# Optimization experiments

Hardware: AMD Instinct MI355X
Metric: run time of the kernel (lower is better)

## Reference

```python
import jax, jax.numpy as jnp
import numpy as np

HS = 1024          # hidden_size
NH_ATTN = 16       # attention heads
NH_LACT = 4        # lact fast-weight heads
DIN = HS // NH_LACT  # 256
DH = DIN             # inter_multi = 1
CHUNK = 1024       # lact_chunk_size
EPS = 1e-5


def setup_inputs() -> dict:
    key = jax.random.key(0)
    ks = jax.random.split(key, 6)
    B, S = 1, 4096
    x = jax.random.normal(ks[0], (B, S, HS), jnp.float32)
    ln_w = jnp.ones((HS,), jnp.float32)
    ln_b = jnp.zeros((HS,), jnp.float32)
    in_proj_w = jax.random.normal(ks[1], (3 * HS, HS), jnp.float32) * (HS ** -0.5)
    in_proj_b = jnp.zeros((3 * HS,), jnp.float32)
    out_proj_w = jax.random.normal(ks[2], (HS, HS), jnp.float32) * (HS ** -0.5)
    out_proj_b = jnp.zeros((HS,), jnp.float32)
    w0 = jax.random.normal(ks[3], (NH_LACT, DH, DIN), jnp.float32) / np.sqrt(DIN)
    w1 = jax.random.normal(ks[4], (NH_LACT, DIN, DH), jnp.float32) / np.sqrt(DH)
    w2 = jax.random.normal(ks[5], (NH_LACT, DH, DIN), jnp.float32) / np.sqrt(DIN)
    return dict(x=x, ln_w=ln_w, ln_b=ln_b, in_proj_w=in_proj_w, in_proj_b=in_proj_b,
                out_proj_w=out_proj_w, out_proj_b=out_proj_b, w0=w0, w1=w1, w2=w2)


def reference(x, ln_w, ln_b, in_proj_w, in_proj_b, out_proj_w, out_proj_b, w0, w1, w2):
    B, S, D = x.shape
    # LayerNorm
    mu = jnp.mean(x, axis=-1, keepdims=True)
    var = jnp.var(x, axis=-1, keepdims=True)
    xn = (x - mu) * jax.lax.rsqrt(var + EPS) * ln_w + ln_b

    # --- torch nn.MultiheadAttention(batch_first=True), self-attention, no mask ---
    qkv = xn @ in_proj_w.T + in_proj_b                      # [B,S,3D]
    q, k, v = jnp.split(qkv, 3, axis=-1)
    hd = D // NH_ATTN
    def heads(t):
        return t.reshape(B, S, NH_ATTN, hd).transpose(0, 2, 1, 3)  # [B,H,S,hd]
    q = heads(q) * (hd ** -0.5)
    k = heads(k)
    v = heads(v)
    attn = jax.nn.softmax(jnp.einsum('bhqd,bhkd->bhqk', q, k), axis=-1)
    ao = jnp.einsum('bhqk,bhkd->bhqd', attn, v).transpose(0, 2, 1, 3).reshape(B, S, D)
    attn_out = ao @ out_proj_w.T + out_proj_b

    # --- chunked fast-weight SwiGLU TTT (block_causal_lact_swiglu) ---
    # q=k=v=chunk; lr0=lr1=lr2=1; each outer chunk is one TTT step starting from
    # the module parameters: update weights on (k,v) then apply to q (block-causal).
    nc = S // CHUNK
    c = xn.reshape(B, nc, CHUNK, NH_LACT, DIN).transpose(0, 1, 3, 2, 4)  # [B,nc,nh,C,din]
    kv = c  # k == v == q == chunk

    # fast-weight SwiGLU forward on keys: f(k) = w1 @ (silu(w0 k) * (w2 k))
    gate = jnp.einsum('bnhcd,hed->bnhce', kv, w0)     # [B,nc,nh,C,dh]
    sg = jax.nn.sigmoid(gate)
    h = gate * sg                                     # silu
    g = jnp.einsum('bnhcd,hed->bnhce', kv, w2)
    hidden = h * g

    # negative dot-product loss L = -sum(v * f(k)) -> dOut = -v
    dout = -kv                                        # [B,nc,nh,C,din]
    dhid = jnp.einsum('bnhcd,hde->bnhce', dout, w1)
    dh = dhid * g
    dg = dhid * h
    dpre = dh * (sg + gate * sg * (1.0 - sg))         # silu'
    dw1 = jnp.einsum('bnhcd,bnhce->bnhde', dout, hidden)
    dw0 = jnp.einsum('bnhce,bnhcd->bnhed', dpre, kv)
    dw2 = jnp.einsum('bnhce,bnhcd->bnhed', dg, kv)

    # SGD step (lr = 1)
    w0n = w0 - dw0   # [B,nc,nh,dh,din]
    w1n = w1 - dw1
    w2n = w2 - dw2

    # apply updated fast weights to queries
    gq = jnp.einsum('bnhcd,bnhed->bnhce', c, w0n)
    hq = gq * jax.nn.sigmoid(gq)
    gq2 = jnp.einsum('bnhcd,bnhed->bnhce', c, w2n)
    oq = jnp.einsum('bnhce,bnhde->bnhcd', hq * gq2, w1n)  # [B,nc,nh,C,din]
    lact_out = oq.transpose(0, 1, 3, 2, 4).reshape(B, S, D)

    return lact_out + attn_out
```

## Files before the change

kernel.cpp:

```cpp
#include <hip/hip_runtime.h>
#include <hip/hip_bf16.h>


typedef __bf16 bf16_t;
typedef __bf16 bf16x8 __attribute__((ext_vector_type(8)));
typedef __bf16 bf16x4 __attribute__((ext_vector_type(4)));
typedef float  f32x4  __attribute__((ext_vector_type(4)));
typedef float  f32x16 __attribute__((ext_vector_type(16)));

#define SW64(r,cg) ((cg) ^ ((r)&7))
#define SW32(r,cg) ((cg) ^ (((r)>>2)&3))

static __device__ __forceinline__ f32x4 mfma16(bf16x8 a, bf16x8 b, f32x4 c){
  return __builtin_amdgcn_mfma_f32_16x16x32_bf16(a, b, c, 0, 0, 0);
}
static __device__ __forceinline__ f32x16 mfma32(bf16x8 a, bf16x8 b, f32x16 c){
  return __builtin_amdgcn_mfma_f32_32x32x16_bf16(a, b, c, 0, 0, 0);
}
__device__ __forceinline__ float sigm(float x){ return 1.0f/(1.0f + __expf(-x)); }
static __device__ __forceinline__ unsigned pkbf(float lo, float hi){
  unsigned short a = __builtin_bit_cast(unsigned short, (__bf16)lo);
  unsigned short b = __builtin_bit_cast(unsigned short, (__bf16)hi);
  return (unsigned)a | ((unsigned)b<<16);
}

__global__ __launch_bounds__(256) void ln_kernel(const float* __restrict__ x,
    const float* __restrict__ w, const float* __restrict__ b,
    bf16_t* __restrict__ xnb)
{
  int s = blockIdx.x, t = threadIdx.x;
  const float4* xr = (const float4*)(x + (size_t)s*1024);
  float4 v = xr[t];
  float sum = v.x+v.y+v.z+v.w;
  float ss  = v.x*v.x+v.y*v.y+v.z*v.z+v.w*v.w;
  #pragma unroll
  for (int o=32;o>0;o>>=1){ sum += __shfl_down(sum,o); ss += __shfl_down(ss,o); }
  __shared__ float red[8];
  __shared__ float stats[2];
  int wid=t>>6, lane=t&63;
  if(lane==0){ red[wid]=sum; red[4+wid]=ss; }
  __syncthreads();
  if(t==0){
    float S0=red[0]+red[1]+red[2]+red[3];
    float Q0=red[4]+red[5]+red[6]+red[7];
    float mu=S0*(1.0f/1024.0f);
    float var=Q0*(1.0f/1024.0f)-mu*mu;
    stats[0]=mu; stats[1]=rsqrtf(var+1e-5f);
  }
  __syncthreads();
  float mu=stats[0], rs=stats[1];
  float4 wv=((const float4*)w)[t], bv=((const float4*)b)[t];
  float4 o;
  o.x=(v.x-mu)*rs*wv.x+bv.x;
  o.y=(v.y-mu)*rs*wv.y+bv.y;
  o.z=(v.z-mu)*rs*wv.z+bv.z;
  o.w=(v.w-mu)*rs*wv.w+bv.w;
  bf16x4 ob = { (bf16_t)o.x, (bf16_t)o.y, (bf16_t)o.z, (bf16_t)o.w };
  *(bf16x4*)&xnb[(size_t)s*1024 + t*4] = ob;
}

__global__ __launch_bounds__(256) void prep_weights(
  const float* __restrict__ ipw, const float* __restrict__ opw,
  const float* __restrict__ w0, const float* __restrict__ w2,
  const float* __restrict__ w1,
  bf16_t* __restrict__ ipwb, bf16_t* __restrict__ opwb,
  bf16_t* __restrict__ w0b, bf16_t* __restrict__ w2b, bf16_t* __restrict__ w1tb)
{
  long i = ((long)blockIdx.x*256 + threadIdx.x)*4;
  if (i < 3145728) {
    float4 v = *(const float4*)(ipw + i);
    bf16x4 o = {(bf16_t)v.x,(bf16_t)v.y,(bf16_t)v.z,(bf16_t)v.w};
    *(bf16x4*)&ipwb[i] = o;
  } else if (i < 4194304) {
    long j = i - 3145728;
    float4 v = *(const float4*)(opw + j);
    bf16x4 o = {(bf16_t)v.x,(bf16_t)v.y,(bf16_t)v.z,(bf16_t)v.w};
    *(bf16x4*)&opwb[j] = o;
  } else if (i < 4456448) {
    long j = i - 4194304;
    float4 v = *(const float4*)(w0 + j);
    bf16x4 o = {(bf16_t)v.x,(bf16_t)v.y,(bf16_t)v.z,(bf16_t)v.w};
    *(bf16x4*)&w0b[j] = o;
  } else if (i < 4718592) {
    long j = i - 4456448;
    float4 v = *(const float4*)(w2 + j);
    bf16x4 o = {(bf16_t)v.x,(bf16_t)v.y,(bf16_t)v.z,(bf16_t)v.w};
    *(bf16x4*)&w2b[j] = o;
  } else if (i < 4980736) {
    long j = i - 4718592;
    int h = (int)(j>>16), rem = (int)(j&65535), d = rem>>8, e0 = rem&255;
    float4 v = *(const float4*)(w1 + j);
    bf16_t* dst = w1tb + h*65536 + d;
    dst[(e0+0)*256] = (bf16_t)v.x;
    dst[(e0+1)*256] = (bf16_t)v.y;
    dst[(e0+2)*256] = (bf16_t)v.z;
    dst[(e0+3)*256] = (bf16_t)v.w;
  }
}

__global__ __launch_bounds__(256) void xnT_kernel(const bf16_t* __restrict__ xnb,
                                                  bf16_t* __restrict__ xt)
{
  int dt = blockIdx.x, ct = blockIdx.y, bz = blockIdx.z;
  int nb = bz>>2, hb = bz&3;
  int t = threadIdx.x;
  __shared__ __align__(16) bf16_t T[4096];
  int r = t>>2, seg = t&3;
  const bf16_t* src = xnb + ((size_t)nb*1024 + ct*64 + r)*1024 + hb*256 + dt*64 + seg*16;
  uint4 a0 = *(const uint4*)src;
  uint4 a1 = *(const uint4*)(src + 8);
  *(uint4*)&T[r*64 + ((((seg*2  )&7)^(r&7))<<3)] = a0;
  *(uint4*)&T[r*64 + ((((seg*2+1)&7)^(r&7))<<3)] = a1;
  __syncthreads();
  int d = t>>2, s2 = t&3;
  unsigned uu[8];
  #pragma unroll
  for (int p=0;p<8;p++){
    int c0 = s2*16 + 2*p, c1 = c0+1;
    unsigned short e0 = __builtin_bit_cast(unsigned short,
        T[c0*64 + (((d>>3)^(c0&7))<<3) + (d&7)]);
    unsigned short e1 = __builtin_bit_cast(unsigned short,
        T[c1*64 + (((d>>3)^(c1&7))<<3) + (d&7)]);
    uu[p] = (unsigned)e0 | ((unsigned)e1<<16);
  }
  uint4 o0 = {uu[0],uu[1],uu[2],uu[3]}, o1 = {uu[4],uu[5],uu[6],uu[7]};
  bf16_t* dst = xt + (size_t)bz*262144 + (size_t)(dt*64 + d)*1024 + ct*64 + s2*16;
  *(uint4*)dst = o0;
  *(uint4*)(dst+8) = o1;
}

template<int EPI>
__global__ __launch_bounds__(256) void gemm_mfma(
  const bf16_t* __restrict__ Ag, const bf16_t* __restrict__ Bg,
  float* __restrict__ Cg, const float* __restrict__ bias,
  bf16_t* __restrict__ O1, bf16_t* __restrict__ O2, bf16_t* __restrict__ O3,
  int M, int N, int K, int lda, int ldb, int ldc,
  long oAn, long oAh, long oBn, long oBh, long oCn, long oCh)
{
  int bz = blockIdx.z, nb = bz>>2, hb = bz&3;
  const bf16_t* A = Ag + (long)nb*oAn + (long)hb*oAh;
  const bf16_t* B = Bg + (long)nb*oBn + (long)hb*oBh;
  int m0 = blockIdx.y<<7, n0 = blockIdx.x<<7;
  int t = threadIdx.x, l = t&63, w = t>>6;
  int wr = w>>1, wc = w&1;
  __shared__ __align__(16) bf16_t As[4096], Bs[4096];
  f32x4 acc[4][4];
  #pragma unroll
  for (int i=0;i<4;i++)
    #pragma unroll
    for (int j=0;j<4;j++){ f32x4 z={0.f,0.f,0.f,0.f}; acc[i][j]=z; }

  int r0 = t>>2, c0 = t&3, r1 = r0+64;
  const bf16_t* Arow0 = A + (size_t)(m0+r0)*lda + c0*8;
  const bf16_t* Arow1 = A + (size_t)(m0+r1)*lda + c0*8;
  const bf16_t* Brow0 = B + (size_t)(n0+r0)*ldb + c0*8;
  const bf16_t* Brow1 = B + (size_t)(n0+r1)*ldb + c0*8;
  uint4 av0 = *(const uint4*)Arow0, av1 = *(const uint4*)Arow1;
  uint4 bv0 = *(const uint4*)Brow0, bv1 = *(const uint4*)Brow1;
  int wo0 = r0*32 + (SW32(r0,c0)<<3), wo1 = r1*32 + (SW32(r1,c0)<<3);

  for (int k0=0; k0<K; k0+=32) {
    if (k0) __syncthreads();
    *(uint4*)&As[wo0] = av0; *(uint4*)&As[wo1] = av1;
    *(uint4*)&Bs[wo0] = bv0; *(uint4*)&Bs[wo1] = bv1;
    __syncthreads();
    if (k0+32 < K) {
      av0 = *(const uint4*)(Arow0 + k0+32); av1 = *(const uint4*)(Arow1 + k0+32);
      bv0 = *(const uint4*)(Brow0 + k0+32); bv1 = *(const uint4*)(Brow1 + k0+32);
    }
    bf16x8 af[4], bb[4];
    #pragma unroll
    for (int mt=0;mt<4;mt++){
      int row = (wr<<6)+(mt<<4)+(l&15);
      af[mt] = *(bf16x8*)&As[row*32 + (SW32(row, (l>>4))<<3)];
    }
    #pragma unroll
    for (int nt=0;nt<4;nt++){
      int row = (wc<<6)+(nt<<4)+(l&15);
      bb[nt] = *(bf16x8*)&Bs[row*32 + (SW32(row, (l>>4))<<3)];
    }
    #pragma unroll
    for (int mt=0;mt<4;mt++)
      #pragma unroll
      for (int nt=0;nt<4;nt++)
        acc[mt][nt] = mfma16(af[mt], bb[nt], acc[mt][nt]);
  }

  float* C = Cg + (long)nb*oCn + (long)hb*oCh;
  #pragma unroll
  for (int mt=0;mt<4;mt++){
    #pragma unroll
    for (int nt=0;nt<4;nt++){
      #pragma unroll
      for (int q=0;q<4;q++){
        int gr = m0 + (wr<<6) + (mt<<4) + ((l>>4)<<2) + q;
        int gc = n0 + (wc<<6) + (nt<<4) + (l&15);
        float v = acc[mt][nt][q];
        if constexpr (EPI==0) {
          C[(size_t)gr*ldc + gc] = v;
        } else if constexpr (EPI==1) {
          C[(size_t)gr*ldc + gc] = v + bias[gc];
        } else if constexpr (EPI==2) {
          C[(size_t)gr*ldc + gc] += v;
        } else if constexpr (EPI==3) {
          v += bias[gc];
          int seg = gc>>10, c2 = gc&1023, hh = c2>>6, dd = c2&63;
          size_t oi = ((size_t)hh*4096 + gr)*64 + dd;
          if (seg==0)      O1[oi] = (bf16_t)(v*0.18033688011112042f);
          else if (seg==1) O2[oi] = (bf16_t)v;
          else             O3[oi] = (bf16_t)v;
        } else {
          float pv = bias[(long)hb*65536 + (size_t)gr*256 + gc];
          float r = (EPI==4) ? (pv + v) : (pv - v);
          O1[(long)bz*65536 + (size_t)gr*256 + gc] = (bf16_t)r;
        }
      }
    }
  }
}

__global__ __launch_bounds__(256) void vtrans(const bf16_t* __restrict__ Vb,
                                              bf16_t* __restrict__ Vt)
{
  int st = blockIdx.x, h = blockIdx.y, t = threadIdx.x;
  __shared__ __align__(16) bf16_t T[64*72];
  #pragma unroll
  for (int G=t; G<512; G+=256) {
    int r = G>>3, cg = G&7;
    *(uint4*)&T[r*72 + cg*8] =
      *(const uint4*)(Vb + ((size_t)h*4096 + st*64 + r)*64 + cg*8);
  }
  __syncthreads();
  int d = t>>2, seg = t&3;
  bf16x8 e0, e1;
  #pragma unroll
  for (int i=0;i<8;i++)  e0[i] = T[(seg*16+i)*72 + d];
  #pragma unroll
  for (int i=0;i<8;i++)  e1[i] = T[(seg*16+8+i)*72 + d];
  size_t base = ((size_t)h*64 + d)*4096 + st*64 + seg*16;
  *(bf16x8*)(Vt + base)     = e0;
  *(bf16x8*)(Vt + base + 8) = e1;
}

__global__ __launch_bounds__(256,2) void attn_mfma2(
    const bf16_t* __restrict__ Qb, const bf16_t* __restrict__ Kb,
    const bf16_t* __restrict__ Vt, bf16_t* __restrict__ ao)
{
  int h = blockIdx.x, qblk = blockIdx.y;
  int t = threadIdx.x, w = t>>6, l = t&63;
  int lh = l>>5, lq = l&31;
  __shared__ __align__(16) bf16_t Ks[4096], Vs[4096];

  const bf16_t* Kg = Kb + (size_t)h*4096*64;
  const bf16_t* Vg = Vt + (size_t)h*64*4096;

  bf16x8 qf[4];
  {
    const bf16_t* Qg = Qb + ((size_t)h*4096 + (size_t)qblk*128 + w*32 + lq)*64 + lh*8;
    #pragma unroll
    for (int s=0;s<4;s++) qf[s] = *(const bf16x8*)(Qg + s*16);
  }

  int r0 = t>>3, c0 = t&7, r1 = r0+32;
  uint4 kv0 = *(const uint4*)(Kg + (size_t)r0*64 + c0*8);
  uint4 kv1 = *(const uint4*)(Kg + (size_t)r1*64 + c0*8);
  uint4 vv0 = *(const uint4*)(Vg + (size_t)r0*4096 + c0*8);
  uint4 vv1 = *(const uint4*)(Vg + (size_t)r1*4096 + c0*8);

  float m_r = -1e30f, l_r = 0.f;
  f32x16 Oa, Ob;
  #pragma unroll
  for (int i=0;i<16;i++){ Oa[i]=0.f; Ob[i]=0.f; }

  int wo0 = r0*64 + (SW64(r0,c0)<<3);
  int wo1 = r1*64 + (SW64(r1,c0)<<3);

  for (int kt=0; kt<64; ++kt) {
    __syncthreads();
    *(uint4*)&Ks[wo0] = kv0;
    *(uint4*)&Ks[wo1] = kv1;
    *(uint4*)&Vs[wo0] = vv0;
    *(uint4*)&Vs[wo1] = vv1;
    __syncthreads();
    if (kt < 63) {
      const bf16_t* Kg2 = Kg + (size_t)(kt+1)*4096;
      kv0 = *(const uint4*)(Kg2 + (size_t)r0*64 + c0*8);
      kv1 = *(const uint4*)(Kg2 + (size_t)r1*64 + c0*8);
      const bf16_t* Vg2 = Vg + (kt+1)*64;
      vv0 = *(const uint4*)(Vg2 + (size_t)r0*4096 + c0*8);
      vv1 = *(const uint4*)(Vg2 + (size_t)r1*4096 + c0*8);
    }
    f32x16 S0, S1;
    #pragma unroll
    for (int i=0;i<16;i++){ S0[i]=0.f; S1[i]=0.f; }
    #pragma unroll
    for (int s=0;s<4;s++){
      int g = (s<<1) + lh;
      bf16x8 k0 = *(const bf16x8*)&Ks[lq*64 + (SW64(lq,g)<<3)];
      int rowb = 32 + lq;
      bf16x8 k1 = *(const bf16x8*)&Ks[rowb*64 + (SW64(rowb,g)<<3)];
      S0 = mfma32(k0, qf[s], S0);
      S1 = mfma32(k1, qf[s], S1);
    }
    float mx = S0[0];
    #pragma unroll
    for (int i=1;i<16;i++) mx = fmaxf(mx, S0[i]);
    #pragma unroll
    for (int i=0;i<16;i++) mx = fmaxf(mx, S1[i]);
    mx = fmaxf(mx, __shfl_xor(mx, 32));
    if (__any(mx > m_r + 8.0f)) {
      float mn = fmaxf(m_r, mx);
      float sc = exp2f(m_r - mn);
      l_r *= sc;
      m_r = mn;
      #pragma unroll
      for (int reg=0; reg<16; reg++){
        int row = (reg&3) + 8*(reg>>2) + 4*lh;
        float s_row = __shfl(sc, row);
        Oa[reg] *= s_row;
        Ob[reg] *= s_row;
      }
    }
    float rs = 0.f;
    #pragma unroll
    for (int i=0;i<16;i++){ float p = exp2f(S0[i]-m_r); S0[i]=p; rs+=p; }
    #pragma unroll
    for (int i=0;i<16;i++){ float p = exp2f(S1[i]-m_r); S1[i]=p; rs+=p; }
    rs += __shfl_xor(rs, 32);
    l_r += rs;
    unsigned pk0[4][2], pk1[4][2];
    #pragma unroll
    for (int u2=0; u2<4; u2++){
      #pragma unroll
      for (int wd=0; wd<2; wd++){
        int q0 = 4*u2 + 2*wd;
        pk0[u2][wd] = pkbf(S0[q0], S0[q0+1]);
        pk1[u2][wd] = pkbf(S1[q0], S1[q0+1]);
      }
    }
    #pragma unroll
    for (int ks=0; ks<4; ks++){
      int v0 = 2*(ks&1);
      unsigned x0, x1, y0, y1;
      if (ks < 2) { x0 = pk0[v0][0]; x1 = pk0[v0][1]; y0 = pk0[v0+1][0]; y1 = pk0[v0+1][1]; }
      else        { x0 = pk1[v0][0]; x1 = pk1[v0][1]; y0 = pk1[v0+1][0]; y1 = pk1[v0+1][1]; }
      asm volatile("v_permlane32_swap_b32 %0, %1" : "+v"(x0), "+v"(y0));
      asm volatile("v_permlane32_swap_b32 %0, %1" : "+v"(x1), "+v"(y1));
      uint4 pau = {x0, x1, y0, y1};
      bf16x8 pa = __builtin_bit_cast(bf16x8, pau);
      int g = (ks<<1) + lh;
      bf16x8 vf0 = *(const bf16x8*)&Vs[lq*64 + (SW64(lq,g)<<3)];
      int rowb = 32 + lq;
      bf16x8 vf1 = *(const bf16x8*)&Vs[rowb*64 + (SW64(rowb,g)<<3)];
      Oa = mfma32(pa, vf0, Oa);
      Ob = mfma32(pa, vf1, Ob);
    }
  }
  #pragma unroll
  for (int reg=0; reg<16; reg++){
    int row = (reg&3) + 8*(reg>>2) + 4*lh;
    float lr = __shfl(l_r, row);
    float inv = 1.0f/lr;
    int grow = qblk*128 + w*32 + row;
    size_t base = (size_t)grow*1024 + h*64;
    ao[base + lq]      = (bf16_t)(Oa[reg]*inv);
    ao[base + 32 + lq] = (bf16_t)(Ob[reg]*inv);
  }
}

__global__ __launch_bounds__(256) void ew1T_kernel(
    const float* __restrict__ b0, const float* __restrict__ b1,
    const float* __restrict__ b2,
    bf16_t* __restrict__ hT, bf16_t* __restrict__ pT, bf16_t* __restrict__ gT)
{
  int et = blockIdx.x, ct = blockIdx.y, bz = blockIdx.z;
  int t = threadIdx.x;
  __shared__ __align__(16) bf16_t Th[4096], Tp[4096], Tg[4096];
  int r = t>>2, seg = t&3;
  size_t base = (size_t)bz*262144 + (size_t)(ct*64 + r)*256 + et*64 + seg*16;
  unsigned ph[8], pp[8], pg[8];
  #pragma unroll
  for (int j=0;j<4;j++){
    float4 gate = *(const float4*)(b0 + base + j*4);
    float4 gg   = *(const float4*)(b1 + base + j*4);
    float4 dh   = *(const float4*)(b2 + base + j*4);
    float hid[4], dpre[4], dgv[4];
    #define EW(c,idx) { float sg=sigm(gate.c); float hs=gate.c*sg; hid[idx]=hs*gg.c; \
                        float nd=-dh.c; float dh_=nd*gg.c; \
                        dpre[idx]=dh_*(sg+gate.c*sg*(1.0f-sg)); dgv[idx]=nd*hs; }
    EW(x,0) EW(y,1) EW(z,2) EW(w,3)
    #undef EW
    ph[j*2  ] = pkbf(hid[0],  hid[1]);  ph[j*2+1] = pkbf(hid[2],  hid[3]);
    pp[j*2  ] = pkbf(dpre[0], dpre[1]); pp[j*2+1] = pkbf(dpre[2], dpre[3]);
    pg[j*2  ] = pkbf(dgv[0],  dgv[1]);  pg[j*2+1] = pkbf(dgv[2],  dgv[3]);
  }
  int g0 = ((seg*2  )&7)^(r&7), g1 = ((seg*2+1)&7)^(r&7);
  uint4 h0={ph[0],ph[1],ph[2],ph[3]}, h1={ph[4],ph[5],ph[6],ph[7]};
  uint4 p0={pp[0],pp[1],pp[2],pp[3]}, p1={pp[4],pp[5],pp[6],pp[7]};
  uint4 q0={pg[0],pg[1],pg[2],pg[3]}, q1={pg[4],pg[5],pg[6],pg[7]};
  *(uint4*)&Th[r*64 + (g0<<3)] = h0; *(uint4*)&Th[r*64 + (g1<<3)] = h1;
  *(uint4*)&Tp[r*64 + (g0<<3)] = p0; *(uint4*)&Tp[r*64 + (g1<<3)] = p1;
  *(uint4*)&Tg[r*64 + (g0<<3)] = q0; *(uint4*)&Tg[r*64 + (g1<<3)] = q1;
  __syncthreads();
  int e = t>>2, s2 = t&3;
  size_t obase = (size_t)bz*262144 + (size_t)(et*64 + e)*1024 + ct*64 + s2*16;
  #pragma unroll
  for (int tens=0; tens<3; tens++){
    const bf16_t* T = (tens==0)?Th:(tens==1)?Tp:Tg;
    bf16_t* dst = ((tens==0)?hT:(tens==1)?pT:gT) + obase;
    unsigned uu[8];
    #pragma unroll
    for (int p=0;p<8;p++){
      int c0 = s2*16 + 2*p, c1 = c0+1;
      unsigned short e0 = __builtin_bit_cast(unsigned short,
          T[c0*64 + (((e>>3)^(c0&7))<<3) + (e&7)]);
      unsigned short e1 = __builtin_bit_cast(unsigned short,
          T[c1*64 + (((e>>3)^(c1&7))<<3) + (e&7)]);
      uu[p] = (unsigned)e0 | ((unsigned)e1<<16);
    }
    uint4 o0 = {uu[0],uu[1],uu[2],uu[3]}, o1 = {uu[4],uu[5],uu[6],uu[7]};
    *(uint4*)dst = o0;
    *(uint4*)(dst+8) = o1;
  }
}

__global__ __launch_bounds__(256) void lact_ew2(const float* __restrict__ gq,
    const float* __restrict__ gq2, bf16_t* __restrict__ ub)
{
  int i=blockIdx.x*256+threadIdx.x;
  float4 a=((const float4*)gq)[i], b=((const float4*)gq2)[i];
  bf16x4 o;
  o[0]=(bf16_t)(a.x*sigm(a.x)*b.x);
  o[1]=(bf16_t)(a.y*sigm(a.y)*b.y);
  o[2]=(bf16_t)(a.z*sigm(a.z)*b.z);
  o[3]=(bf16_t)(a.w*sigm(a.w)*b.w);
  *(bf16x4*)&ub[(size_t)i*4]=o;
}

extern "C" void kernel_launch(void* const* d_in, const int* in_sizes, int n_in,
                              void* d_out, int out_size, void* d_ws, size_t ws_size,
                              hipStream_t stream) {
  const float* x          = (const float*)d_in[0];
  const float* ln_w       = (const float*)d_in[1];
  const float* ln_b       = (const float*)d_in[2];
  const float* in_proj_w  = (const float*)d_in[3];
  const float* in_proj_b  = (const float*)d_in[4];
  const float* out_proj_w = (const float*)d_in[5];
  const float* out_proj_b = (const float*)d_in[6];
  const float* w0         = (const float*)d_in[7];
  const float* w1         = (const float*)d_in[8];
  const float* w2         = (const float*)d_in[9];
  float* out = (float*)d_out;

  float* ws = (float*)d_ws;
  bf16_t* xnb  = (bf16_t*)(ws);
  bf16_t* Qb   = (bf16_t*)(ws + 2097152);
  bf16_t* Kb   = (bf16_t*)(ws + 4194304);
  float*  buf0 = ws + 6291456;
  float*  buf1 = ws + 10485760;
  float*  buf2 = ws + 14680064;
  bf16_t* xnTb = (bf16_t*)(ws + 18874368);
  bf16_t* hTb  = (bf16_t*)(ws + 20971520);
  bf16_t* pTb  = (bf16_t*)(ws + 23068672);
  bf16_t* gTb  = (bf16_t*)(ws + 25165824);
  bf16_t* ipwb = (bf16_t*)(ws + 27262976);
  bf16_t* opwb = (bf16_t*)(ws + 28835840);
  bf16_t* w0b  = (bf16_t*)(ws + 29360128);
  bf16_t* w2b  = (bf16_t*)(ws + 29491200);
  bf16_t* w1tb = (bf16_t*)(ws + 29622272);
  bf16_t* w0nb = (bf16_t*)(ws + 29753344);
  bf16_t* w1nb = (bf16_t*)(ws + 30277632);
  bf16_t* w2nb = (bf16_t*)(ws + 30801920);
  bf16_t* Vb   = (bf16_t*)buf0;
  bf16_t* aob  = (bf16_t*)buf1;
  bf16_t* Vtp  = (bf16_t*)buf2;
  bf16_t* ub   = (bf16_t*)buf2;

  dim3 blk(256);

  ln_kernel<<<dim3(4096),blk,0,stream>>>(x, ln_w, ln_b, xnb);

  prep_weights<<<dim3(4864),blk,0,stream>>>(in_proj_w, out_proj_w, w0, w2, w1,
                                            ipwb, opwb, w0b, w2b, w1tb);

  gemm_mfma<3><<<dim3(24,32,1),blk,0,stream>>>(
      xnb, ipwb, nullptr, in_proj_b, Qb, Kb, Vb,
      4096,3072,1024, 1024,1024,0, 0,0,0,0,0,0);

  vtrans<<<dim3(64,16),blk,0,stream>>>(Vb, Vtp);

  attn_mfma2<<<dim3(16,32),blk,0,stream>>>(Qb, Kb, Vtp, aob);

  gemm_mfma<1><<<dim3(8,32,1),blk,0,stream>>>(
      aob, opwb, out, out_proj_b, nullptr,nullptr,nullptr,
      4096,1024,1024, 1024,1024,1024, 0,0,0,0,0,0);

  xnT_kernel<<<dim3(4,16,16),blk,0,stream>>>(xnb, xnTb);

  gemm_mfma<0><<<dim3(2,8,16),blk,0,stream>>>(
      xnb, w0b, buf0, nullptr, nullptr,nullptr,nullptr,
      1024,256,256, 1024,256,256, 1048576,256, 0,65536, 1048576,262144);
  gemm_mfma<0><<<dim3(2,8,16),blk,0,stream>>>(
      xnb, w2b, buf1, nullptr, nullptr,nullptr,nullptr,
      1024,256,256, 1024,256,256, 1048576,256, 0,65536, 1048576,262144);
  gemm_mfma<0><<<dim3(2,8,16),blk,0,stream>>>(
      xnb, w1tb, buf2, nullptr, nullptr,nullptr,nullptr,
      1024,256,256, 1024,256,256, 1048576,256, 0,65536, 1048576,262144);

  ew1T_kernel<<<dim3(4,16,16),blk,0,stream>>>(buf0, buf1, buf2, hTb, pTb, gTb);

  gemm_mfma<4><<<dim3(2,2,16),blk,0,stream>>>(
      xnTb, hTb, nullptr, w1, w1nb, nullptr,nullptr,
      256,256,1024, 1024,1024,0, 1048576,262144, 1048576,262144, 0,0);
  gemm_mfma<5><<<dim3(2,2,16),blk,0,stream>>>(
      pTb, xnTb, nullptr, w0, w0nb, nullptr,nullptr,
      256,256,1024, 1024,1024,0, 1048576,262144, 1048576,262144, 0,0);
  gemm_mfma<5><<<dim3(2,2,16),blk,0,stream>>>(
      gTb, xnTb, nullptr, w2, w2nb, nullptr,nullptr,
      256,256,1024, 1024,1024,0, 1048576,262144, 1048576,262144, 0,0);

  gemm_mfma<0><<<dim3(2,8,16),blk,0,stream>>>(
      xnb, w0nb, buf0, nullptr, nullptr,nullptr,nullptr,
      1024,256,256, 1024,256,256, 1048576,256, 262144,65536, 1048576,262144);
  gemm_mfma<0><<<dim3(2,8,16),blk,0,stream>>>(
      xnb, w2nb, buf1, nullptr, nullptr,nullptr,nullptr,
      1024,256,256, 1024,256,256, 1048576,256, 262144,65536, 1048576,262144);

  lact_ew2<<<dim3(4096),blk,0,stream>>>(buf0, buf1, ub);

  gemm_mfma<2><<<dim3(2,8,16),blk,0,stream>>>(
      ub, w1nb, out, nullptr, nullptr,nullptr,nullptr,
      1024,256,256, 256,256,1024, 1048576,262144, 262144,65536, 1048576,256);
}
```

Measured before the change: 448.8 us.

## Split attention over key halves with merge, batch LaCT GEMMs, fuse SwiGLU into final GEMM

Result: faster. 397.1 us (-11.5%).

```diff
diff --git a/kernel.cpp b/kernel.cpp
--- a/kernel.cpp
+++ b/kernel.cpp
@@ -22,6 +22,16 @@
   unsigned short a = __builtin_bit_cast(unsigned short, (__bf16)lo);
   unsigned short b = __builtin_bit_cast(unsigned short, (__bf16)hi);
   return (unsigned)a | ((unsigned)b<<16);
+}
+static __device__ __forceinline__ float hswap_max(float x){
+  float a=x, b=x;
+  asm volatile("v_permlane32_swap_b32 %0, %1" : "+v"(a), "+v"(b));
+  return fmaxf(a,b);
+}
+static __device__ __forceinline__ float hswap_add(float x){
+  float a=x, b=x;
+  asm volatile("v_permlane32_swap_b32 %0, %1" : "+v"(a), "+v"(b));
+  return a+b;
 }
 
 __global__ __launch_bounds__(256) void ln_kernel(const float* __restrict__ x,
@@ -129,34 +139,53 @@
   *(uint4*)(dst+8) = o1;
 }
 
-template<int EPI>
-__global__ __launch_bounds__(256) void gemm_mfma(
-  const bf16_t* __restrict__ Ag, const bf16_t* __restrict__ Bg,
-  float* __restrict__ Cg, const float* __restrict__ bias,
-  bf16_t* __restrict__ O1, bf16_t* __restrict__ O2, bf16_t* __restrict__ O3,
-  int M, int N, int K, int lda, int ldb, int ldc,
-  long oAn, long oAh, long oBn, long oBh, long oCn, long oCh)
-{
-  int bz = blockIdx.z, nb = bz>>2, hb = bz&3;
-  const bf16_t* A = Ag + (long)nb*oAn + (long)hb*oAh;
-  const bf16_t* B = Bg + (long)nb*oBn + (long)hb*oBh;
-  int m0 = blockIdx.y<<7, n0 = blockIdx.x<<7;
-  int t = threadIdx.x, l = t&63, w = t>>6;
-  int wr = w>>1, wc = w&1;
+template<bool AEW>
+__device__ __forceinline__ void gemm_core(
+    const bf16_t* __restrict__ A, const float* __restrict__ F0,
+    const float* __restrict__ F1, int lda,
+    const bf16_t* __restrict__ B, int ldb,
+    int K, int m0, int n0, f32x4 (&acc)[4][4])
+{
+  int t = threadIdx.x, l = t&63;
+  int w = t>>6, wr = w>>1, wc = w&1;
   __shared__ __align__(16) bf16_t As[4096], Bs[4096];
-  f32x4 acc[4][4];
-  #pragma unroll
-  for (int i=0;i<4;i++)
-    #pragma unroll
-    for (int j=0;j<4;j++){ f32x4 z={0.f,0.f,0.f,0.f}; acc[i][j]=z; }
-
   int r0 = t>>2, c0 = t&3, r1 = r0+64;
-  const bf16_t* Arow0 = A + (size_t)(m0+r0)*lda + c0*8;
-  const bf16_t* Arow1 = A + (size_t)(m0+r1)*lda + c0*8;
+  const bf16_t* Arow0 = nullptr; const bf16_t* Arow1 = nullptr;
+  const float *Fa0=nullptr,*Fa1=nullptr,*Fb0=nullptr,*Fb1=nullptr;
+  if constexpr (AEW) {
+    Fa0 = F0 + (size_t)(m0+r0)*lda + c0*8;
+    Fa1 = F0 + (size_t)(m0+r1)*lda + c0*8;
+    Fb0 = F1 + (size_t)(m0+r0)*lda + c0*8;
+    Fb1 = F1 + (size_t)(m0+r1)*lda + c0*8;
+  } else {
+    Arow0 = A + (size_t)(m0+r0)*lda + c0*8;
+    Arow1 = A + (size_t)(m0+r1)*lda + c0*8;
+  }
   const bf16_t* Brow0 = B + (size_t)(n0+r0)*ldb + c0*8;
   const bf16_t* Brow1 = B + (size_t)(n0+r1)*ldb + c0*8;
-  uint4 av0 = *(const uint4*)Arow0, av1 = *(const uint4*)Arow1;
-  uint4 bv0 = *(const uint4*)Brow0, bv1 = *(const uint4*)Brow1;
+
+  uint4 av0, av1, bv0, bv1;
+  auto loadA = [&](int k0, uint4& o0, uint4& o1){
+    if constexpr (AEW) {
+      float4 ga = *(const float4*)(Fa0 + k0), gb = *(const float4*)(Fa0 + k0 + 4);
+      float4 ha = *(const float4*)(Fb0 + k0), hb = *(const float4*)(Fb0 + k0 + 4);
+      o0.x = pkbf(ga.x*sigm(ga.x)*ha.x, ga.y*sigm(ga.y)*ha.y);
+      o0.y = pkbf(ga.z*sigm(ga.z)*ha.z, ga.w*sigm(ga.w)*ha.w);
+      o0.z = pkbf(gb.x*sigm(gb.x)*hb.x, gb.y*sigm(gb.y)*hb.y);
+      o0.w = pkbf(gb.z*sigm(gb.z)*hb.z, gb.w*sigm(gb.w)*hb.w);
+      float4 gc = *(const float4*)(Fa1 + k0), gd = *(const float4*)(Fa1 + k0 + 4);
+      float4 hc = *(const float4*)(Fb1 + k0), hd = *(const float4*)(Fb1 + k0 + 4);
+      o1.x = pkbf(gc.x*sigm(gc.x)*hc.x, gc.y*sigm(gc.y)*hc.y);
+      o1.y = pkbf(gc.z*sigm(gc.z)*hc.z, gc.w*sigm(gc.w)*hc.w);
+      o1.z = pkbf(gd.x*sigm(gd.x)*hd.x, gd.y*sigm(gd.y)*hd.y);
+      o1.w = pkbf(gd.z*sigm(gd.z)*hd.z, gd.w*sigm(gd.w)*hd.w);
+    } else {
+      o0 = *(const uint4*)(Arow0 + k0);
+      o1 = *(const uint4*)(Arow1 + k0);
+    }
+  };
+  loadA(0, av0, av1);
+  bv0 = *(const uint4*)Brow0; bv1 = *(const uint4*)Brow1;
   int wo0 = r0*32 + (SW32(r0,c0)<<3), wo1 = r1*32 + (SW32(r1,c0)<<3);
 
   for (int k0=0; k0<K; k0+=32) {
@@ -165,7 +194,7 @@
     *(uint4*)&Bs[wo0] = bv0; *(uint4*)&Bs[wo1] = bv1;
     __syncthreads();
     if (k0+32 < K) {
-      av0 = *(const uint4*)(Arow0 + k0+32); av1 = *(const uint4*)(Arow1 + k0+32);
+      loadA(k0+32, av0, av1);
       bv0 = *(const uint4*)(Brow0 + k0+32); bv1 = *(const uint4*)(Brow1 + k0+32);
     }
     bf16x8 af[4], bb[4];
@@ -185,38 +214,105 @@
       for (int nt=0;nt<4;nt++)
         acc[mt][nt] = mfma16(af[mt], bb[nt], acc[mt][nt]);
   }
-
-  float* C = Cg + (long)nb*oCn + (long)hb*oCh;
-  #pragma unroll
-  for (int mt=0;mt<4;mt++){
-    #pragma unroll
-    for (int nt=0;nt<4;nt++){
-      #pragma unroll
-      for (int q=0;q<4;q++){
-        int gr = m0 + (wr<<6) + (mt<<4) + ((l>>4)<<2) + q;
-        int gc = n0 + (wc<<6) + (nt<<4) + (l&15);
-        float v = acc[mt][nt][q];
-        if constexpr (EPI==0) {
-          C[(size_t)gr*ldc + gc] = v;
-        } else if constexpr (EPI==1) {
-          C[(size_t)gr*ldc + gc] = v + bias[gc];
-        } else if constexpr (EPI==2) {
-          C[(size_t)gr*ldc + gc] += v;
-        } else if constexpr (EPI==3) {
-          v += bias[gc];
-          int seg = gc>>10, c2 = gc&1023, hh = c2>>6, dd = c2&63;
-          size_t oi = ((size_t)hh*4096 + gr)*64 + dd;
-          if (seg==0)      O1[oi] = (bf16_t)(v*0.18033688011112042f);
-          else if (seg==1) O2[oi] = (bf16_t)v;
-          else             O3[oi] = (bf16_t)v;
-        } else {
-          float pv = bias[(long)hb*65536 + (size_t)gr*256 + gc];
-          float r = (EPI==4) ? (pv + v) : (pv - v);
-          O1[(long)bz*65536 + (size_t)gr*256 + gc] = (bf16_t)r;
-        }
-      }
-    }
-  }
+}
+
+#define EPILOOP(...) { int l=threadIdx.x&63, w_=threadIdx.x>>6, wr=w_>>1, wc=w_&1; \
+  _Pragma("unroll") for(int mt=0;mt<4;mt++) _Pragma("unroll") for(int nt=0;nt<4;nt++) \
+  _Pragma("unroll") for(int q=0;q<4;q++){ \
+    int gr=m0+(wr<<6)+(mt<<4)+((l>>4)<<2)+q; int gc=n0+(wc<<6)+(nt<<4)+(l&15); \
+    float v=acc[mt][nt][q]; __VA_ARGS__ } }
+
+#define ACCZERO f32x4 acc[4][4]; \
+  _Pragma("unroll") for(int i_=0;i_<4;i_++) _Pragma("unroll") for(int j_=0;j_<4;j_++){ \
+    f32x4 z_={0.f,0.f,0.f,0.f}; acc[i_][j_]=z_; }
+
+template<int EPI>
+__global__ __launch_bounds__(256) void gemm_big(
+  const bf16_t* __restrict__ A, const bf16_t* __restrict__ B,
+  float* __restrict__ C, const float* __restrict__ bias,
+  bf16_t* __restrict__ O1, bf16_t* __restrict__ O2, bf16_t* __restrict__ O3,
+  int K, int ldc)
+{
+  int m0 = blockIdx.y<<7, n0 = blockIdx.x<<7;
+  ACCZERO
+  gemm_core<false>(A, nullptr, nullptr, K, B, K, K, m0, n0, acc);
+  EPILOOP(
+    if constexpr (EPI==1) {
+      C[(size_t)gr*ldc + gc] = v + bias[gc];
+    } else {
+      v += bias[gc];
+      int seg = gc>>10; int c2 = gc&1023; int hh = c2>>6; int dd = c2&63;
+      size_t oi = ((size_t)hh*4096 + gr)*64 + dd;
+      if (seg==0)      O1[oi] = (bf16_t)(v*0.18033688011112042f);
+      else if (seg==1) O2[oi] = (bf16_t)v;
+      else             O3[oi] = (bf16_t)v;
+    }
+  )
+}
+
+__global__ __launch_bounds__(256) void lact_fwd(
+    const bf16_t* __restrict__ xnb,
+    const bf16_t* __restrict__ w0b, const bf16_t* __restrict__ w2b,
+    const bf16_t* __restrict__ w1tb,
+    float* __restrict__ b0, float* __restrict__ b1, float* __restrict__ b2)
+{
+  int bz = blockIdx.z, sel = blockIdx.x>>1;
+  const bf16_t* A = xnb + (size_t)(bz>>2)*1048576 + (size_t)(bz&3)*256;
+  const bf16_t* B = (sel==0?w0b:(sel==1?w2b:w1tb)) + (size_t)(bz&3)*65536;
+  float* C = (sel==0?b0:(sel==1?b1:b2)) + (size_t)bz*262144;
+  int m0 = blockIdx.y<<7, n0 = (blockIdx.x&1)<<7;
+  ACCZERO
+  gemm_core<false>(A, nullptr, nullptr, 1024, B, 256, 256, m0, n0, acc);
+  EPILOOP( C[(size_t)gr*256 + gc] = v; )
+}
+
+__global__ __launch_bounds__(256) void lact_apply(
+    const bf16_t* __restrict__ xnb,
+    const bf16_t* __restrict__ w0nb, const bf16_t* __restrict__ w2nb,
+    float* __restrict__ b0, float* __restrict__ b1)
+{
+  int bz = blockIdx.z, sel = blockIdx.x>>1;
+  const bf16_t* A = xnb + (size_t)(bz>>2)*1048576 + (size_t)(bz&3)*256;
+  const bf16_t* B = (sel? w2nb : w0nb) + (size_t)bz*65536;
+  float* C = (sel? b1 : b0) + (size_t)bz*262144;
+  int m0 = blockIdx.y<<7, n0 = (blockIdx.x&1)<<7;
+  ACCZERO
+  gemm_core<false>(A, nullptr, nullptr, 1024, B, 256, 256, m0, n0, acc);
+  EPILOOP( C[(size_t)gr*256 + gc] = v; )
+}
+
+__global__ __launch_bounds__(256) void lact_upd(
+    const bf16_t* __restrict__ xnTb, const bf16_t* __restrict__ hTb,
+    const bf16_t* __restrict__ pTb,  const bf16_t* __restrict__ gTb,
+    const float* __restrict__ w1, const float* __restrict__ w0,
+    const float* __restrict__ w2,
+    bf16_t* __restrict__ w1nb, bf16_t* __restrict__ w0nb, bf16_t* __restrict__ w2nb)
+{
+  int zz = blockIdx.z, sub = zz>>4, bz = zz&15, hb = bz&3;
+  const bf16_t* A = (sub==0? xnTb : (sub==1? pTb : gTb)) + (size_t)bz*262144;
+  const bf16_t* B = (sub==0? hTb : xnTb) + (size_t)bz*262144;
+  const float*  P = (sub==0? w1 : (sub==1? w0 : w2)) + (size_t)hb*65536;
+  bf16_t*       O = (sub==0? w1nb : (sub==1? w0nb : w2nb)) + (size_t)bz*65536;
+  float sgn = (sub==0) ? 1.0f : -1.0f;
+  int m0 = blockIdx.y<<7, n0 = blockIdx.x<<7;
+  ACCZERO
+  gemm_core<false>(A, nullptr, nullptr, 1024, B, 1024, 1024, m0, n0, acc);
+  EPILOOP( O[(size_t)gr*256 + gc] = (bf16_t)(P[(size_t)gr*256 + gc] + sgn*v); )
+}
+
+__global__ __launch_bounds__(256) void lact_final(
+    const float* __restrict__ gq, const float* __restrict__ gq2,
+    const bf16_t* __restrict__ w1nb, float* __restrict__ out)
+{
+  int bz = blockIdx.z;
+  const float* F0 = gq  + (size_t)bz*262144;
+  const float* F1 = gq2 + (size_t)bz*262144;
+  const bf16_t* B = w1nb + (size_t)bz*65536;
+  float* C = out + (size_t)(bz>>2)*1048576 + (size_t)(bz&3)*256;
+  int m0 = blockIdx.y<<7, n0 = (blockIdx.x&1)<<7;
+  ACCZERO
+  gemm_core<true>(nullptr, F0, F1, 256, B, 256, 256, m0, n0, acc);
+  EPILOOP( C[(size_t)gr*1024 + gc] += v; )
 }
 
 __global__ __launch_bounds__(256) void vtrans(const bf16_t* __restrict__ Vb,
@@ -242,17 +338,18 @@
   *(bf16x8*)(Vt + base + 8) = e1;
 }
 
-__global__ __launch_bounds__(256,2) void attn_mfma2(
+__global__ __launch_bounds__(256,4) void attn_mfma3(
     const bf16_t* __restrict__ Qb, const bf16_t* __restrict__ Kb,
-    const bf16_t* __restrict__ Vt, bf16_t* __restrict__ ao)
-{
-  int h = blockIdx.x, qblk = blockIdx.y;
+    const bf16_t* __restrict__ Vt, float* __restrict__ Opart,
+    float* __restrict__ mlpart)
+{
+  int h = blockIdx.x, qblk = blockIdx.y, z = blockIdx.z;
   int t = threadIdx.x, w = t>>6, l = t&63;
   int lh = l>>5, lq = l&31;
   __shared__ __align__(16) bf16_t Ks[4096], Vs[4096];
 
-  const bf16_t* Kg = Kb + (size_t)h*4096*64;
-  const bf16_t* Vg = Vt + (size_t)h*64*4096;
+  const bf16_t* Kg = Kb + (size_t)h*262144 + (size_t)z*131072;
+  const bf16_t* Vg = Vt + (size_t)h*262144 + (size_t)z*2048;
 
   bf16x8 qf[4];
   {
@@ -275,14 +372,14 @@
   int wo0 = r0*64 + (SW64(r0,c0)<<3);
   int wo1 = r1*64 + (SW64(r1,c0)<<3);
 
-  for (int kt=0; kt<64; ++kt) {
+  for (int kt=0; kt<32; ++kt) {
     __syncthreads();
     *(uint4*)&Ks[wo0] = kv0;
     *(uint4*)&Ks[wo1] = kv1;
     *(uint4*)&Vs[wo0] = vv0;
     *(uint4*)&Vs[wo1] = vv1;
     __syncthreads();
-    if (kt < 63) {
+    if (kt < 31) {
       const bf16_t* Kg2 = Kg + (size_t)(kt+1)*4096;
       kv0 = *(const uint4*)(Kg2 + (size_t)r0*64 + c0*8);
       kv1 = *(const uint4*)(Kg2 + (size_t)r1*64 + c0*8);
@@ -293,6 +390,7 @@
     f32x16 S0, S1;
     #pragma unroll
     for (int i=0;i<16;i++){ S0[i]=0.f; S1[i]=0.f; }
+    __builtin_amdgcn_s_setprio(1);
     #pragma unroll
     for (int s=0;s<4;s++){
       int g = (s<<1) + lh;
@@ -302,12 +400,14 @@
       S0 = mfma32(k0, qf[s], S0);
       S1 = mfma32(k1, qf[s], S1);
     }
-    float mx = S0[0];
-    #pragma unroll
-    for (int i=1;i<16;i++) mx = fmaxf(mx, S0[i]);
-    #pragma unroll
-    for (int i=0;i<16;i++) mx = fmaxf(mx, S1[i]);
-    mx = fmaxf(mx, __shfl_xor(mx, 32));
+    __builtin_amdgcn_s_setprio(0);
+    float mt_[8];
+    #pragma unroll
+    for (int i=0;i<8;i++) mt_[i] = fmaxf(fmaxf(S0[i],S0[i+8]), fmaxf(S1[i],S1[i+8]));
+    #pragma unroll
+    for (int i=0;i<4;i++) mt_[i] = fmaxf(mt_[i], mt_[i+4]);
+    float mx = fmaxf(fmaxf(mt_[0],mt_[1]), fmaxf(mt_[2],mt_[3]));
+    mx = hswap_max(mx);
     if (__any(mx > m_r + 8.0f)) {
       float mn = fmaxf(m_r, mx);
       float sc = exp2f(m_r - mn);
@@ -321,13 +421,17 @@
         Ob[reg] *= s_row;
       }
     }
-    float rs = 0.f;
-    #pragma unroll
-    for (int i=0;i<16;i++){ float p = exp2f(S0[i]-m_r); S0[i]=p; rs+=p; }
-    #pragma unroll
-    for (int i=0;i<16;i++){ float p = exp2f(S1[i]-m_r); S1[i]=p; rs+=p; }
-    rs += __shfl_xor(rs, 32);
-    l_r += rs;
+    #pragma unroll
+    for (int i=0;i<16;i++) S0[i] = exp2f(S0[i]-m_r);
+    #pragma unroll
+    for (int i=0;i<16;i++) S1[i] = exp2f(S1[i]-m_r);
+    float rt[8];
+    #pragma unroll
+    for (int i=0;i<8;i++) rt[i] = (S0[i]+S0[i+8]) + (S1[i]+S1[i+8]);
+    #pragma unroll
+    for (int i=0;i<4;i++) rt[i] += rt[i+4];
+    float rs = (rt[0]+rt[1])+(rt[2]+rt[3]);
+    l_r += hswap_add(rs);
     unsigned pk0[4][2], pk1[4][2];
     #pragma unroll
     for (int u2=0; u2<4; u2++){
@@ -338,6 +442,7 @@
         pk1[u2][wd] = pkbf(S1[q0], S1[q0+1]);
       }
     }
+    __builtin_amdgcn_s_setprio(1);
     #pragma unroll
     for (int ks=0; ks<4; ks++){
       int v0 = 2*(ks&1);
@@ -355,16 +460,49 @@
       Oa = mfma32(pa, vf0, Oa);
       Ob = mfma32(pa, vf1, Ob);
     }
-  }
+    __builtin_amdgcn_s_setprio(0);
+  }
+  size_t pb = ((size_t)(h*32+qblk))*2 + z;
+  float* Op = Opart + pb*8192 + (size_t)(w*32)*64;
   #pragma unroll
   for (int reg=0; reg<16; reg++){
     int row = (reg&3) + 8*(reg>>2) + 4*lh;
-    float lr = __shfl(l_r, row);
-    float inv = 1.0f/lr;
-    int grow = qblk*128 + w*32 + row;
-    size_t base = (size_t)grow*1024 + h*64;
-    ao[base + lq]      = (bf16_t)(Oa[reg]*inv);
-    ao[base + 32 + lq] = (bf16_t)(Ob[reg]*inv);
+    Op[row*64 + lq]      = Oa[reg];
+    Op[row*64 + 32 + lq] = Ob[reg];
+  }
+  if (l < 32) {
+    *(float2*)&mlpart[pb*256 + (size_t)(w*32+l)*2] = float2{m_r, l_r};
+  }
+}
+
+__global__ __launch_bounds__(256) void attn_merge(
+    const float* __restrict__ Opart, const float* __restrict__ mlpart,
+    bf16_t* __restrict__ ao)
+{
+  int h = blockIdx.x, qblk = blockIdx.y, t = threadIdx.x;
+  int r = t>>1, ch = (t&1)<<5;
+  size_t b = ((size_t)(h*32+qblk))*2;
+  const float* O0 = Opart + b*8192;
+  const float* O1 = O0 + 8192;
+  float2 v0 = ((const float2*)(mlpart + b*256))[r];
+  float2 v1 = ((const float2*)(mlpart + b*256 + 256))[r];
+  float M = fmaxf(v0.x, v1.x);
+  float a0 = exp2f(v0.x - M), a1 = exp2f(v1.x - M);
+  float inv = 1.0f/(v0.y*a0 + v1.y*a1);
+  float s0 = a0*inv, s1 = a1*inv;
+  bf16_t* dst = ao + (size_t)(qblk*128+r)*1024 + h*64 + ch;
+  const float* p0 = O0 + r*64 + ch;
+  const float* p1 = O1 + r*64 + ch;
+  #pragma unroll
+  for (int j=0;j<8;j++){
+    float4 o0 = *(const float4*)(p0 + j*4);
+    float4 o1 = *(const float4*)(p1 + j*4);
+    bf16x4 ov;
+    ov[0]=(bf16_t)(o0.x*s0+o1.x*s1);
+    ov[1]=(bf16_t)(o0.y*s0+o1.y*s1);
+    ov[2]=(bf16_t)(o0.z*s0+o1.z*s1);
+    ov[3]=(bf16_t)(o0.w*s0+o1.w*s1);
+    *(bf16x4*)(dst + j*4) = ov;
   }
 }
 
@@ -422,19 +560,6 @@
     *(uint4*)dst = o0;
     *(uint4*)(dst+8) = o1;
   }
-}
-
-__global__ __launch_bounds__(256) void lact_ew2(const float* __restrict__ gq,
-    const float* __restrict__ gq2, bf16_t* __restrict__ ub)
-{
-  int i=blockIdx.x*256+threadIdx.x;
-  float4 a=((const float4*)gq)[i], b=((const float4*)gq2)[i];
-  bf16x4 o;
-  o[0]=(bf16_t)(a.x*sigm(a.x)*b.x);
-  o[1]=(bf16_t)(a.y*sigm(a.y)*b.y);
-  o[2]=(bf16_t)(a.z*sigm(a.z)*b.z);
-  o[3]=(bf16_t)(a.w*sigm(a.w)*b.w);
-  *(bf16x4*)&ub[(size_t)i*4]=o;
 }
 
 extern "C" void kernel_launch(void* const* d_in, const int* in_sizes, int n_in,
@@ -463,7 +588,9 @@
   bf16_t* hTb  = (bf16_t*)(ws + 20971520);
   bf16_t* pTb  = (bf16_t*)(ws + 23068672);
   bf16_t* gTb  = (bf16_t*)(ws + 25165824);
+  float*  Opart= ws + 18874368;
   bf16_t* ipwb = (bf16_t*)(ws + 27262976);
+  float*  mlp  = ws + 27262976;
   bf16_t* opwb = (bf16_t*)(ws + 28835840);
   bf16_t* w0b  = (bf16_t*)(ws + 29360128);
   bf16_t* w2b  = (bf16_t*)(ws + 29491200);
@@ -474,7 +601,6 @@
   bf16_t* Vb   = (bf16_t*)buf0;
   bf16_t* aob  = (bf16_t*)buf1;
   bf16_t* Vtp  = (bf16_t*)buf2;
-  bf16_t* ub   = (bf16_t*)buf2;
 
   dim3 blk(256);
 
@@ -483,52 +609,28 @@
   prep_weights<<<dim3(4864),blk,0,stream>>>(in_proj_w, out_proj_w, w0, w2, w1,
                                             ipwb, opwb, w0b, w2b, w1tb);
 
-  gemm_mfma<3><<<dim3(24,32,1),blk,0,stream>>>(
-      xnb, ipwb, nullptr, in_proj_b, Qb, Kb, Vb,
-      4096,3072,1024, 1024,1024,0, 0,0,0,0,0,0);
+  gemm_big<3><<<dim3(24,32),blk,0,stream>>>(
+      xnb, ipwb, nullptr, in_proj_b, Qb, Kb, Vb, 1024, 0);
 
   vtrans<<<dim3(64,16),blk,0,stream>>>(Vb, Vtp);
 
-  attn_mfma2<<<dim3(16,32),blk,0,stream>>>(Qb, Kb, Vtp, aob);
-
-  gemm_mfma<1><<<dim3(8,32,1),blk,0,stream>>>(
-      aob, opwb, out, out_proj_b, nullptr,nullptr,nullptr,
-      4096,1024,1024, 1024,1024,1024, 0,0,0,0,0,0);
+  attn_mfma3<<<dim3(16,32,2),blk,0,stream>>>(Qb, Kb, Vtp, Opart, mlp);
+
+  attn_merge<<<dim3(16,32),blk,0,stream>>>(Opart, mlp, aob);
+
+  gemm_big<1><<<dim3(8,32),blk,0,stream>>>(
+      aob, opwb, out, out_proj_b, nullptr,nullptr,nullptr, 1024, 1024);
 
   xnT_kernel<<<dim3(4,16,16),blk,0,stream>>>(xnb, xnTb);
 
-  gemm_mfma<0><<<dim3(2,8,16),blk,0,stream>>>(
-      xnb, w0b, buf0, nullptr, nullptr,nullptr,nullptr,
-      1024,256,256, 1024,256,256, 1048576,256, 0,65536, 1048576,262144);
-  gemm_mfma<0><<<dim3(2,8,16),blk,0,stream>>>(
-      xnb, w2b, buf1, nullptr, nullptr,nullptr,nullptr,
-      1024,256,256, 1024,256,256, 1048576,256, 0,65536, 1048576,262144);
-  gemm_mfma<0><<<dim3(2,8,16),blk,0,stream>>>(
-      xnb, w1tb, buf2, nullptr, nullptr,nullptr,nullptr,
-      1024,256,256, 1024,256,256, 1048576,256, 0,65536, 1048576,262144);
+  lact_fwd<<<dim3(6,8,16),blk,0,stream>>>(xnb, w0b, w2b, w1tb, buf0, buf1, buf2);
 
   ew1T_kernel<<<dim3(4,16,16),blk,0,stream>>>(buf0, buf1, buf2, hTb, pTb, gTb);
 
-  gemm_mfma<4><<<dim3(2,2,16),blk,0,stream>>>(
-      xnTb, hTb, nullptr, w1, w1nb, nullptr,nullptr,
-      256,256,1024, 1024,1024,0, 1048576,262144, 1048576,262144, 0,0);
-  gemm_mfma<5><<<dim3(2,2,16),blk,0,stream>>>(
-      pTb, xnTb, nullptr, w0, w0nb, nullptr,nullptr,
-      256,256,1024, 1024,1024,0, 1048576,262144, 1048576,262144, 0,0);
-  gemm_mfma<5><<<dim3(2,2,16),blk,0,stream>>>(
-      gTb, xnTb, nullptr, w2, w2nb, nullptr,nullptr,
-      256,256,1024, 1024,1024,0, 1048576,262144, 1048576,262144, 0,0);
-
-  gemm_mfma<0><<<dim3(2,8,16),blk,0,stream>>>(
-      xnb, w0nb, buf0, nullptr, nullptr,nullptr,nullptr,
-      1024,256,256, 1024,256,256, 1048576,256, 262144,65536, 1048576,262144);
-  gemm_mfma<0><<<dim3(2,8,16),blk,0,stream>>>(
-      xnb, w2nb, buf1, nullptr, nullptr,nullptr,nullptr,
-      1024,256,256, 1024,256,256, 1048576,256, 262144,65536, 1048576,262144);
-
-  lact_ew2<<<dim3(4096),blk,0,stream>>>(buf0, buf1, ub);
-
-  gemm_mfma<2><<<dim3(2,8,16),blk,0,stream>>>(
-      ub, w1nb, out, nullptr, nullptr,nullptr,nullptr,
-      1024,256,256, 256,256,1024, 1048576,262144, 262144,65536, 1048576,256);
-}
+  lact_upd<<<dim3(2,2,48),blk,0,stream>>>(xnTb, hTb, pTb, gTb,
+                                          w1, w0, w2, w1nb, w0nb, w2nb);
+
+  lact_apply<<<dim3(4,8,16),blk,0,stream>>>(xnb, w0nb, w2nb, buf0, buf1);
+
+  lact_final<<<dim3(2,8,16),blk,0,stream>>>(buf0, buf1, w1nb, out);
+}
```
